# Performance work log

Measured on AMD Instinct MI355X. Metric: run time of the kernel, lower is better.

The kernel has to match this reference:

```python
import jax, jax.numpy as jnp
import numpy as np


def _laplacian(c):
    # c: [1, 1, D, H, W]; zero-padded 7-point stencil, identical to
    # F.conv3d with the sparse kernel (+1 on 6 face neighbors, -6 center, padding=1).
    p = jnp.pad(c, ((0, 0), (0, 0), (1, 1), (1, 1), (1, 1)))
    return (p[:, :, 2:, 1:-1, 1:-1] + p[:, :, :-2, 1:-1, 1:-1]
            + p[:, :, 1:-1, 2:, 1:-1] + p[:, :, 1:-1, :-2, 1:-1]
            + p[:, :, 1:-1, 1:-1, 2:] + p[:, :, 1:-1, 1:-1, :-2]
            - 6.0 * c)


def setup_inputs() -> dict:
    key = jax.random.key(0)
    k1, k2, k3 = jax.random.split(key, 3)
    shape = (1, 1, 192, 192, 192)
    c_init = jax.random.uniform(k1, shape, dtype=jnp.float32)
    D_map = jax.random.uniform(k2, shape, dtype=jnp.float32)
    rho_map = jax.random.uniform(k3, shape, dtype=jnp.float32)
    dt = jnp.ones((1,), dtype=jnp.float32)
    return {"c_init": c_init, "D_map": D_map, "rho_map": rho_map, "dt": dt, "steps": 20}


def reference(c_init, D_map, rho_map, dt, steps):
    delta_t = dt[0] / steps

    def body(i, c):
        diffusion = D_map * _laplacian(c)
        reaction = rho_map * c * (1.0 - c)
        c = c + (diffusion + reaction) * delta_t
        return jnp.clip(c, 0.0, 1.0)

    return jax.lax.fori_loop(0, steps, body, c_init)
```

## Files before the change

kernel.cpp:

```cpp
#include <hip/hip_runtime.h>


constexpr int W = 192, H = 192, DZ = 192;
constexpr int PLANE = W * H;
constexpr int NELEM = PLANE * DZ;
constexpr int VW = W / 4;
constexpr int VPLANE = PLANE / 4;
constexpr int YB = 8;
constexpr int YEXT = YB + 2;
constexpr int ZC = 12;
constexpr int ROWF = 200;
constexpr int SLOT = YEXT * ROWF;
constexpr int NT = 512;

__global__ __launch_bounds__(NT) void rd_fused2(
    const float* __restrict__ c,
    const float* __restrict__ Dm,
    const float* __restrict__ rho,
    const float* __restrict__ dt,
    const int* __restrict__ steps,
    float* __restrict__ out)
{
    __shared__ float s1[4 * SLOT];

    const int tid = threadIdx.x;
    const int y0 = blockIdx.x * YB;
    const int z0 = blockIdx.y * ZC;

    const float delta_t = dt[0] / (float)steps[0];

    const float4* __restrict__ c4 = (const float4*)c;
    const float4* __restrict__ D4 = (const float4*)Dm;
    const float4* __restrict__ r4 = (const float4*)rho;
    float4* __restrict__ o4 = (float4*)out;

    const int ty = tid / VW;
    const int tx = tid % VW;
    const bool s1act = (ty < YEXT);
    const int yg  = y0 - 1 + ty;
    const int ygc = min(max(yg, 0), H - 1);
    const float mrow = (yg >= 0 && yg < H) ? 1.f : 0.f;
    const float mym = (yg > 0 && yg < H) ? 1.f : 0.f;
    const float myp = (yg >= 0 && yg < H - 1) ? 1.f : 0.f;
    const int oym = (yg > 0 && yg < H) ? -VW : 0;
    const int oyp = (yg >= 0 && yg < H - 1) ? VW : 0;
    const float mxl = (tx > 0) ? 1.f : 0.f;
    const float mxr = (tx < VW - 1) ? 1.f : 0.f;
    const int oxl = (tx > 0) ? -1 : 0;
    const int oxr = (tx < VW - 1) ? 4 : 3;

    const int rowbase = ygc * VW + tx;
    const int s1off = ty * ROWF + 4 * tx;

    float4 zmr, ccr;
    {
        const int pa = min(max(z0 - 2, 0), DZ - 1);
        const int pb = min(max(z0 - 1, 0), DZ - 1);
        zmr = c4[pa * VPLANE + rowbase];
        ccr = c4[pb * VPLANE + rowbase];
    }

    auto S1 = [&](int p) {
        const int pc  = min(max(p, 0), DZ - 1);
        const int pzp = min(max(p + 1, 0), DZ - 1);
        const float mp  = (p >= 0 && p < DZ) ? mrow : 0.f;
        const float mzm = (p > 0) ? 1.f : 0.f;
        const float mzp = (p < DZ - 1) ? 1.f : 0.f;
        const int bp = pc * VPLANE + rowbase;

        const float4 zp = c4[pzp * VPLANE + rowbase];
        const float4 ym = c4[bp + oym];
        const float4 yp = c4[bp + oyp];
        const float4 Dq = D4[bp];
        const float4 rq = r4[bp];
        const float  xl = c[4 * bp + oxl];
        const float  xr = c[4 * bp + oxr];

        float4 lap;
        lap.x = mxl * xl + ccr.y + mym * ym.x + myp * yp.x
              + mzm * zmr.x + mzp * zp.x - 6.f * ccr.x;
        lap.y = ccr.x + ccr.z + mym * ym.y + myp * yp.y
              + mzm * zmr.y + mzp * zp.y - 6.f * ccr.y;
        lap.z = ccr.y + ccr.w + mym * ym.z + myp * yp.z
              + mzm * zmr.z + mzp * zp.z - 6.f * ccr.z;
        lap.w = ccr.z + mxr * xr + mym * ym.w + myp * yp.w
              + mzm * zmr.w + mzp * zp.w - 6.f * ccr.w;

        float4 v;
        v.x = ccr.x + (Dq.x * lap.x + rq.x * ccr.x * (1.f - ccr.x)) * delta_t;
        v.y = ccr.y + (Dq.y * lap.y + rq.y * ccr.y * (1.f - ccr.y)) * delta_t;
        v.z = ccr.z + (Dq.z * lap.z + rq.z * ccr.z * (1.f - ccr.z)) * delta_t;
        v.w = ccr.w + (Dq.w * lap.w + rq.w * ccr.w * (1.f - ccr.w)) * delta_t;

        v.x = mp * fminf(fmaxf(v.x, 0.f), 1.f);
        v.y = mp * fminf(fmaxf(v.y, 0.f), 1.f);
        v.z = mp * fminf(fmaxf(v.z, 0.f), 1.f);
        v.w = mp * fminf(fmaxf(v.w, 0.f), 1.f);

        *(float4*)&s1[(p & 3) * SLOT + s1off] = v;

        zmr = ccr;
        ccr = zp;
    };

    const int r2 = tid / VW + 1;
    const bool s2act = (tid < YB * VW);
    const int s2off = r2 * ROWF + 4 * tx;
    const int oxl2 = (tx > 0) ? -1 : 0;
    const int oxr2 = (tx < VW - 1) ? 4 : 3;
    const int yout = y0 + r2 - 1;

    if (s1act) { S1(z0 - 1); S1(z0); }

    for (int z = z0; z < z0 + ZC; ++z) {
        if (s1act && (z + 1 < DZ)) S1(z + 1);
        __syncthreads();
        if (s2act) {
            const float* sc = &s1[(z & 3) * SLOT];
            const float* sm = &s1[((z - 1) & 3) * SLOT];
            const float* sp = &s1[((z + 1) & 3) * SLOT];
            const float mzm = (z > 0) ? 1.f : 0.f;
            const float mzp = (z < DZ - 1) ? 1.f : 0.f;

            const float4 cc = *(const float4*)&sc[s2off];
            const float4 ym = *(const float4*)&sc[s2off - ROWF];
            const float4 yp = *(const float4*)&sc[s2off + ROWF];
            const float4 zm = *(const float4*)&sm[s2off];
            const float4 zp = *(const float4*)&sp[s2off];
            const float  xl = sc[s2off + oxl2];
            const float  xr = sc[s2off + oxr2];

            const int gi = z * VPLANE + yout * VW + tx;
            const float4 Dq = D4[gi];
            const float4 rq = r4[gi];

            float4 lap;
            lap.x = mxl * xl + cc.y + ym.x + yp.x
                  + mzm * zm.x + mzp * zp.x - 6.f * cc.x;
            lap.y = cc.x + cc.z + ym.y + yp.y
                  + mzm * zm.y + mzp * zp.y - 6.f * cc.y;
            lap.z = cc.y + cc.w + ym.z + yp.z
                  + mzm * zm.z + mzp * zp.z - 6.f * cc.z;
            lap.w = cc.z + mxr * xr + ym.w + yp.w
                  + mzm * zm.w + mzp * zp.w - 6.f * cc.w;

            float4 v;
            v.x = cc.x + (Dq.x * lap.x + rq.x * cc.x * (1.f - cc.x)) * delta_t;
            v.y = cc.y + (Dq.y * lap.y + rq.y * cc.y * (1.f - cc.y)) * delta_t;
            v.z = cc.z + (Dq.z * lap.z + rq.z * cc.z * (1.f - cc.z)) * delta_t;
            v.w = cc.w + (Dq.w * lap.w + rq.w * cc.w * (1.f - cc.w)) * delta_t;

            v.x = fminf(fmaxf(v.x, 0.f), 1.f);
            v.y = fminf(fmaxf(v.y, 0.f), 1.f);
            v.z = fminf(fmaxf(v.z, 0.f), 1.f);
            v.w = fminf(fmaxf(v.w, 0.f), 1.f);

            o4[gi] = v;
        }
        __syncthreads();
    }
}

extern "C" void kernel_launch(void* const* d_in, const int* in_sizes, int n_in,
                              void* d_out, int out_size, void* d_ws, size_t ws_size,
                              hipStream_t stream) {
    const float* c_init = (const float*)d_in[0];
    const float* Dm     = (const float*)d_in[1];
    const float* rho    = (const float*)d_in[2];
    const float* dt     = (const float*)d_in[3];
    const int*   steps  = (const int*)d_in[4];

    float* bufA = (float*)d_ws;
    float* bufB = bufA + NELEM;
    float* outp = (float*)d_out;

    const int NPAIR = 10;

    dim3 block(NT, 1, 1);
    dim3 grid(H / YB, DZ / ZC, 1);

    const float* src = c_init;
    for (int i = 0; i < NPAIR; ++i) {
        float* dst = (i == NPAIR - 1) ? outp : ((i & 1) ? bufB : bufA);
        rd_fused2<<<grid, block, 0, stream>>>(src, Dm, rho, dt, steps, dst);
        src = dst;
    }
}
```

Measured before the change: 398.0 us.

## Replace z-marching pipeline with small z-blocks and single-barrier two-step fusion

```diff
diff --git a/kernel.cpp b/kernel.cpp
--- a/kernel.cpp
+++ b/kernel.cpp
@@ -8,12 +8,13 @@
 constexpr int VPLANE = PLANE / 4;
 constexpr int YB = 8;
 constexpr int YEXT = YB + 2;
-constexpr int ZC = 12;
+constexpr int ZB = 4;
+constexpr int NS1 = ZB + 2;
 constexpr int ROWF = 200;
 constexpr int SLOT = YEXT * ROWF;
 constexpr int NT = 512;
 
-__global__ __launch_bounds__(NT) void rd_fused2(
+__global__ __launch_bounds__(NT, 6) void rd_fused2(
     const float* __restrict__ c,
     const float* __restrict__ Dm,
     const float* __restrict__ rho,
@@ -21,11 +22,11 @@
     const int* __restrict__ steps,
     float* __restrict__ out)
 {
-    __shared__ float s1[4 * SLOT];
+    __shared__ float s1[NS1 * SLOT];
 
     const int tid = threadIdx.x;
     const int y0 = blockIdx.x * YB;
-    const int z0 = blockIdx.y * ZC;
+    const int z0 = blockIdx.y * ZB;
 
     const float delta_t = dt[0] / (float)steps[0];
 
@@ -36,128 +37,121 @@
 
     const int ty = tid / VW;
     const int tx = tid % VW;
-    const bool s1act = (ty < YEXT);
-    const int yg  = y0 - 1 + ty;
-    const int ygc = min(max(yg, 0), H - 1);
-    const float mrow = (yg >= 0 && yg < H) ? 1.f : 0.f;
-    const float mym = (yg > 0 && yg < H) ? 1.f : 0.f;
-    const float myp = (yg >= 0 && yg < H - 1) ? 1.f : 0.f;
-    const int oym = (yg > 0 && yg < H) ? -VW : 0;
-    const int oyp = (yg >= 0 && yg < H - 1) ? VW : 0;
-    const float mxl = (tx > 0) ? 1.f : 0.f;
-    const float mxr = (tx < VW - 1) ? 1.f : 0.f;
-    const int oxl = (tx > 0) ? -1 : 0;
-    const int oxr = (tx < VW - 1) ? 4 : 3;
 
-    const int rowbase = ygc * VW + tx;
-    const int s1off = ty * ROWF + 4 * tx;
+    if (ty < YEXT) {
+        const int yg  = y0 - 1 + ty;
+        const int ygc = min(max(yg, 0), H - 1);
+        const float mrow = (yg >= 0 && yg < H) ? 1.f : 0.f;
+        const float mym = (yg > 0 && yg < H) ? 1.f : 0.f;
+        const float myp = (yg >= 0 && yg < H - 1) ? 1.f : 0.f;
+        const int oym = (yg > 0 && yg < H) ? -VW : 0;
+        const int oyp = (yg >= 0 && yg < H - 1) ? VW : 0;
+        const float mxl = (tx > 0) ? 1.f : 0.f;
+        const float mxr = (tx < VW - 1) ? 1.f : 0.f;
+        const int oxl = (tx > 0) ? -1 : 0;
+        const int oxr = (tx < VW - 1) ? 4 : 3;
 
-    float4 zmr, ccr;
-    {
-        const int pa = min(max(z0 - 2, 0), DZ - 1);
-        const int pb = min(max(z0 - 1, 0), DZ - 1);
-        zmr = c4[pa * VPLANE + rowbase];
-        ccr = c4[pb * VPLANE + rowbase];
+        const int rowbase = ygc * VW + tx;
+        const int s1off = ty * ROWF + 4 * tx;
+
+        float4 zmr = c4[min(max(z0 - 2, 0), DZ - 1) * VPLANE + rowbase];
+        float4 ccr = c4[min(max(z0 - 1, 0), DZ - 1) * VPLANE + rowbase];
+
+#pragma unroll
+        for (int k = 0; k < NS1; ++k) {
+            const int p = z0 - 1 + k;
+            const int pzp = min(max(p + 1, 0), DZ - 1);
+            const float mp  = (p >= 0 && p < DZ) ? mrow : 0.f;
+            const float mzm = (p > 0) ? 1.f : 0.f;
+            const float mzp = (p < DZ - 1) ? 1.f : 0.f;
+            const int bp = min(max(p, 0), DZ - 1) * VPLANE + rowbase;
+
+            const float4 zp = c4[pzp * VPLANE + rowbase];
+            const float4 ym = c4[bp + oym];
+            const float4 yp = c4[bp + oyp];
+            const float4 Dq = D4[bp];
+            const float4 rq = r4[bp];
+            const float  xl = c[4 * bp + oxl];
+            const float  xr = c[4 * bp + oxr];
+
+            float4 lap;
+            lap.x = mxl * xl + ccr.y + mym * ym.x + myp * yp.x
+                  + mzm * zmr.x + mzp * zp.x - 6.f * ccr.x;
+            lap.y = ccr.x + ccr.z + mym * ym.y + myp * yp.y
+                  + mzm * zmr.y + mzp * zp.y - 6.f * ccr.y;
+            lap.z = ccr.y + ccr.w + mym * ym.z + myp * yp.z
+                  + mzm * zmr.z + mzp * zp.z - 6.f * ccr.z;
+            lap.w = ccr.z + mxr * xr + mym * ym.w + myp * yp.w
+                  + mzm * zmr.w + mzp * zp.w - 6.f * ccr.w;
+
+            float4 v;
+            v.x = ccr.x + (Dq.x * lap.x + rq.x * ccr.x * (1.f - ccr.x)) * delta_t;
+            v.y = ccr.y + (Dq.y * lap.y + rq.y * ccr.y * (1.f - ccr.y)) * delta_t;
+            v.z = ccr.z + (Dq.z * lap.z + rq.z * ccr.z * (1.f - ccr.z)) * delta_t;
+            v.w = ccr.w + (Dq.w * lap.w + rq.w * ccr.w * (1.f - ccr.w)) * delta_t;
+
+            v.x = mp * fminf(fmaxf(v.x, 0.f), 1.f);
+            v.y = mp * fminf(fmaxf(v.y, 0.f), 1.f);
+            v.z = mp * fminf(fmaxf(v.z, 0.f), 1.f);
+            v.w = mp * fminf(fmaxf(v.w, 0.f), 1.f);
+
+            *(float4*)&s1[k * SLOT + s1off] = v;
+
+            zmr = ccr;
+            ccr = zp;
+        }
     }
 
-    auto S1 = [&](int p) {
-        const int pc  = min(max(p, 0), DZ - 1);
-        const int pzp = min(max(p + 1, 0), DZ - 1);
-        const float mp  = (p >= 0 && p < DZ) ? mrow : 0.f;
-        const float mzm = (p > 0) ? 1.f : 0.f;
-        const float mzp = (p < DZ - 1) ? 1.f : 0.f;
-        const int bp = pc * VPLANE + rowbase;
+    __syncthreads();
 
-        const float4 zp = c4[pzp * VPLANE + rowbase];
-        const float4 ym = c4[bp + oym];
-        const float4 yp = c4[bp + oyp];
-        const float4 Dq = D4[bp];
-        const float4 rq = r4[bp];
-        const float  xl = c[4 * bp + oxl];
-        const float  xr = c[4 * bp + oxr];
+#pragma unroll
+    for (int j = 0; j < 3; ++j) {
+        const int id = j * NT + tid;
+        const int zz = id / (YB * VW);
+        const int rem = id - zz * (YB * VW);
+        const int yy = rem / VW;
+        const int xx = rem - yy * VW;
+
+        const float mxl = (xx > 0) ? 1.f : 0.f;
+        const float mxr = (xx < VW - 1) ? 1.f : 0.f;
+        const int oxl = (xx > 0) ? -1 : 0;
+        const int oxr = (xx < VW - 1) ? 4 : 3;
+
+        const float* sc = &s1[(zz + 1) * SLOT];
+        const float* sm = &s1[zz * SLOT];
+        const float* sp = &s1[(zz + 2) * SLOT];
+        const int soff = (yy + 1) * ROWF + 4 * xx;
+
+        const float4 cc = *(const float4*)&sc[soff];
+        const float4 ym = *(const float4*)&sc[soff - ROWF];
+        const float4 yp = *(const float4*)&sc[soff + ROWF];
+        const float4 zm = *(const float4*)&sm[soff];
+        const float4 zp = *(const float4*)&sp[soff];
+        const float  xl = sc[soff + oxl];
+        const float  xr = sc[soff + oxr];
+
+        const int gi = (z0 + zz) * VPLANE + (y0 + yy) * VW + xx;
+        const float4 Dq = D4[gi];
+        const float4 rq = r4[gi];
 
         float4 lap;
-        lap.x = mxl * xl + ccr.y + mym * ym.x + myp * yp.x
-              + mzm * zmr.x + mzp * zp.x - 6.f * ccr.x;
-        lap.y = ccr.x + ccr.z + mym * ym.y + myp * yp.y
-              + mzm * zmr.y + mzp * zp.y - 6.f * ccr.y;
-        lap.z = ccr.y + ccr.w + mym * ym.z + myp * yp.z
-              + mzm * zmr.z + mzp * zp.z - 6.f * ccr.z;
-        lap.w = ccr.z + mxr * xr + mym * ym.w + myp * yp.w
-              + mzm * zmr.w + mzp * zp.w - 6.f * ccr.w;
+        lap.x = mxl * xl + cc.y + ym.x + yp.x + zm.x + zp.x - 6.f * cc.x;
+        lap.y = cc.x + cc.z + ym.y + yp.y + zm.y + zp.y - 6.f * cc.y;
+        lap.z = cc.y + cc.w + ym.z + yp.z + zm.z + zp.z - 6.f * cc.z;
+        lap.w = cc.z + mxr * xr + ym.w + yp.w + zm.w + zp.w - 6.f * cc.w;
 
         float4 v;
-        v.x = ccr.x + (Dq.x * lap.x + rq.x * ccr.x * (1.f - ccr.x)) * delta_t;
-        v.y = ccr.y + (Dq.y * lap.y + rq.y * ccr.y * (1.f - ccr.y)) * delta_t;
-        v.z = ccr.z + (Dq.z * lap.z + rq.z * ccr.z * (1.f - ccr.z)) * delta_t;
-        v.w = ccr.w + (Dq.w * lap.w + rq.w * ccr.w * (1.f - ccr.w)) * delta_t;
+        v.x = cc.x + (Dq.x * lap.x + rq.x * cc.x * (1.f - cc.x)) * delta_t;
+        v.y = cc.y + (Dq.y * lap.y + rq.y * cc.y * (1.f - cc.y)) * delta_t;
+        v.z = cc.z + (Dq.z * lap.z + rq.z * cc.z * (1.f - cc.z)) * delta_t;
+        v.w = cc.w + (Dq.w * lap.w + rq.w * cc.w * (1.f - cc.w)) * delta_t;
 
-        v.x = mp * fminf(fmaxf(v.x, 0.f), 1.f);
-        v.y = mp * fminf(fmaxf(v.y, 0.f), 1.f);
-        v.z = mp * fminf(fmaxf(v.z, 0.f), 1.f);
-        v.w = mp * fminf(fmaxf(v.w, 0.f), 1.f);
+        v.x = fminf(fmaxf(v.x, 0.f), 1.f);
+        v.y = fminf(fmaxf(v.y, 0.f), 1.f);
+        v.z = fminf(fmaxf(v.z, 0.f), 1.f);
+        v.w = fminf(fmaxf(v.w, 0.f), 1.f);
 
-        *(float4*)&s1[(p & 3) * SLOT + s1off] = v;
-
-        zmr = ccr;
-        ccr = zp;
-    };
-
-    const int r2 = tid / VW + 1;
-    const bool s2act = (tid < YB * VW);
-    const int s2off = r2 * ROWF + 4 * tx;
-    const int oxl2 = (tx > 0) ? -1 : 0;
-    const int oxr2 = (tx < VW - 1) ? 4 : 3;
-    const int yout = y0 + r2 - 1;
-
-    if (s1act) { S1(z0 - 1); S1(z0); }
-
-    for (int z = z0; z < z0 + ZC; ++z) {
-        if (s1act && (z + 1 < DZ)) S1(z + 1);
-        __syncthreads();
-        if (s2act) {
-            const float* sc = &s1[(z & 3) * SLOT];
-            const float* sm = &s1[((z - 1) & 3) * SLOT];
-            const float* sp = &s1[((z + 1) & 3) * SLOT];
-            const float mzm = (z > 0) ? 1.f : 0.f;
-            const float mzp = (z < DZ - 1) ? 1.f : 0.f;
-
-            const float4 cc = *(const float4*)&sc[s2off];
-            const float4 ym = *(const float4*)&sc[s2off - ROWF];
-            const float4 yp = *(const float4*)&sc[s2off + ROWF];
-            const float4 zm = *(const float4*)&sm[s2off];
-            const float4 zp = *(const float4*)&sp[s2off];
-            const float  xl = sc[s2off + oxl2];
-            const float  xr = sc[s2off + oxr2];
-
-            const int gi = z * VPLANE + yout * VW + tx;
-            const float4 Dq = D4[gi];
-            const float4 rq = r4[gi];
-
-            float4 lap;
-            lap.x = mxl * xl + cc.y + ym.x + yp.x
-                  + mzm * zm.x + mzp * zp.x - 6.f * cc.x;
-            lap.y = cc.x + cc.z + ym.y + yp.y
-                  + mzm * zm.y + mzp * zp.y - 6.f * cc.y;
-            lap.z = cc.y + cc.w + ym.z + yp.z
-                  + mzm * zm.z + mzp * zp.z - 6.f * cc.z;
-            lap.w = cc.z + mxr * xr + ym.w + yp.w
-                  + mzm * zm.w + mzp * zp.w - 6.f * cc.w;
-
-            float4 v;
-            v.x = cc.x + (Dq.x * lap.x + rq.x * cc.x * (1.f - cc.x)) * delta_t;
-            v.y = cc.y + (Dq.y * lap.y + rq.y * cc.y * (1.f - cc.y)) * delta_t;
-            v.z = cc.z + (Dq.z * lap.z + rq.z * cc.z * (1.f - cc.z)) * delta_t;
-            v.w = cc.w + (Dq.w * lap.w + rq.w * cc.w * (1.f - cc.w)) * delta_t;
-
-            v.x = fminf(fmaxf(v.x, 0.f), 1.f);
-            v.y = fminf(fmaxf(v.y, 0.f), 1.f);
-            v.z = fminf(fmaxf(v.z, 0.f), 1.f);
-            v.w = fminf(fmaxf(v.w, 0.f), 1.f);
-
-            o4[gi] = v;
-        }
-        __syncthreads();
+        o4[gi] = v;
     }
 }
 
@@ -177,7 +171,7 @@
     const int NPAIR = 10;
 
     dim3 block(NT, 1, 1);
-    dim3 grid(H / YB, DZ / ZC, 1);
+    dim3 grid(H / YB, DZ / ZB, 1);
 
     const float* src = c_init;
     for (int i = 0; i < NPAIR; ++i) {
```

Result: slower. 434.2 us (+9.1%).
